# Optimization experiments

Measured on AMD Instinct MI355X. Metric: run time of the kernel, lower is better.

The kernel has to match this reference:

```python
import jax, jax.numpy as jnp
import numpy as np

LN_EPS = 1e-5
SA_EPS = 1e-8
NUM_ITERS = 3

def layer_norm(x, w, b):
    mu = jnp.mean(x, axis=-1, keepdims=True)
    var = jnp.mean((x - mu) ** 2, axis=-1, keepdims=True)
    return (x - mu) / jnp.sqrt(var + LN_EPS) * w + b


def setup_inputs() -> dict:
    key = jax.random.key(0)
    ks = jax.random.split(key, 24)
    B, C, H, W = 128, 256, 32, 32
    D, S, MH, NC = 64, 8, 128, 15
    s = lambda k, shape, scale=0.02: jax.random.normal(k, shape, dtype=jnp.float32) * scale
    inp = {
        "x1": jax.random.normal(ks[0], (B, C, H, W), dtype=jnp.float32),
        "x2": jax.random.normal(ks[1], (B, C, H, W), dtype=jnp.float32),
        # 1x1 convs stored as [out,in]
        "conv1_w": s(ks[2], (D, C)), "conv1_b": jnp.zeros((D,), jnp.float32),
        "conv2_w": s(ks[3], (D, C)), "conv2_b": jnp.zeros((D,), jnp.float32),
        "norm_w": jnp.ones((D,), jnp.float32), "norm_b": jnp.zeros((D,), jnp.float32),
        "ni_w": jnp.ones((D,), jnp.float32), "ni_b": jnp.zeros((D,), jnp.float32),
        "ns_w": jnp.ones((D,), jnp.float32), "ns_b": jnp.zeros((D,), jnp.float32),
        "nm_w": jnp.ones((D,), jnp.float32), "nm_b": jnp.zeros((D,), jnp.float32),
        "slots_mu": s(ks[4], (1, 1, D), 1.0), "slots_log_sigma": s(ks[5], (1, 1, D), 0.1),
        "Wq": s(ks[6], (D, D), 0.1), "Wk": s(ks[7], (D, D), 0.1), "Wv": s(ks[8], (D, D), 0.1),
        "gru_wih": s(ks[9], (3 * D, D), 0.1), "gru_whh": s(ks[10], (3 * D, D), 0.1),
        "gru_bih": jnp.zeros((3 * D,), jnp.float32), "gru_bhh": jnp.zeros((3 * D,), jnp.float32),
        "mlp_w1": s(ks[11], (MH, D), 0.1), "mlp_b1": jnp.zeros((MH,), jnp.float32),
        "mlp_w2": s(ks[12], (D, MH), 0.1), "mlp_b2": jnp.zeros((D,), jnp.float32),
        "head_w": s(ks[13], (NC, D), 0.1), "head_b": jnp.zeros((NC,), jnp.float32),
        "noise": jax.random.normal(ks[14], (B, S, D), dtype=jnp.float32),
    }
    return inp


def _forward(x1, x2, conv1_w, conv1_b, conv2_w, conv2_b, norm_w, norm_b,
             ni_w, ni_b, ns_w, ns_b, nm_w, nm_b, slots_mu, slots_log_sigma,
             Wq, Wk, Wv, gru_wih, gru_whh, gru_bih, gru_bhh,
             mlp_w1, mlp_b1, mlp_w2, mlp_b2, head_w, head_b, noise):
    B = x1.shape[0]
    D = Wq.shape[0]
    # 1x1 convs then flatten to tokens: [B, H*W, D]
    t1 = jnp.einsum('bchw,dc->bhwd', x1, conv1_w).reshape(B, -1, D) + conv1_b
    t2 = jnp.einsum('bchw,dc->bhwd', x2, conv2_w).reshape(B, -1, D) + conv2_b
    inputs = jnp.concatenate([t1, t2], axis=1)          # [B, N, D]
    inputs = layer_norm(inputs, norm_w, norm_b)

    # SlotAttention
    inputs = layer_norm(inputs, ni_w, ni_b)
    k = inputs @ Wk.T                                    # [B, N, D]
    v = inputs @ Wv.T
    slots = slots_mu + jnp.exp(slots_log_sigma) * noise  # [B, S, D]
    scale = D ** -0.5
    for _ in range(NUM_ITERS):
        slots_prev = slots
        sn = layer_norm(slots, ns_w, ns_b)
        q = (sn @ Wq.T) * scale                          # [B, S, D]
        attn_logits = jnp.einsum('bnd,bsd->bns', k, q)   # [B, N, S]
        attn = jax.nn.softmax(attn_logits, axis=-1) + SA_EPS
        attn = attn / jnp.sum(attn, axis=-2, keepdims=True)
        updates = jnp.einsum('bns,bnd->bsd', attn, v)    # [B, S, D]
        # GRUCell (torch gate order: r, z, n)
        gi = updates @ gru_wih.T + gru_bih               # [B, S, 3D]
        gh = slots_prev @ gru_whh.T + gru_bhh
        ir, iz, inn = jnp.split(gi, 3, axis=-1)
        hr, hz, hn = jnp.split(gh, 3, axis=-1)
        r = jax.nn.sigmoid(ir + hr)
        z = jax.nn.sigmoid(iz + hz)
        n = jnp.tanh(inn + r * hn)
        slots = (1.0 - z) * n + z * slots_prev
        # residual MLP
        h = layer_norm(slots, nm_w, nm_b)
        h = jax.nn.relu(h @ mlp_w1.T + mlp_b1) @ mlp_w2.T + mlp_b2
        slots = slots + h

    fused = jnp.mean(slots, axis=1)                      # [B, D]
    return fused @ head_w.T + head_b                     # [B, n_classes]


def reference(x1, x2, conv1_w, conv1_b, conv2_w, conv2_b, norm_w, norm_b,
              ni_w, ni_b, ns_w, ns_b, nm_w, nm_b, slots_mu, slots_log_sigma,
              Wq, Wk, Wv, gru_wih, gru_whh, gru_bih, gru_bhh,
              mlp_w1, mlp_b1, mlp_w2, mlp_b2, head_w, head_b, noise):
    return _forward(x1, x2, conv1_w, conv1_b, conv2_w, conv2_b, norm_w, norm_b,
                    ni_w, ni_b, ns_w, ns_b, nm_w, nm_b, slots_mu, slots_log_sigma,
                    Wq, Wk, Wv, gru_wih, gru_whh, gru_bih, gru_bhh,
                    mlp_w1, mlp_b1, mlp_w2, mlp_b2, head_w, head_b, noise)
```

## Files before the change

kernel.cpp:

```cpp
#include <hip/hip_runtime.h>
#include <stdint.h>


typedef __bf16 bf16;
typedef __bf16 bf16x8 __attribute__((ext_vector_type(8)));
typedef float  f32x4  __attribute__((ext_vector_type(4)));

#define MFMA16(a, b, c) __builtin_amdgcn_mfma_f32_16x16x32_bf16((a), (b), (c), 0, 0, 0)

#define ASYNC_LDS16(g, l) \
  __builtin_amdgcn_global_load_lds((const __attribute__((address_space(1))) void*)(g), \
                                   (__attribute__((address_space(3))) void*)(l), 16, 0, 0)

__global__ __launch_bounds__(256) void k0_convert(
    const float* __restrict__ c1w, const float* __restrict__ c2w,
    const float* __restrict__ wk,  const float* __restrict__ wvv,
    bf16* __restrict__ wconv, bf16* __restrict__ wkv)
{
  const int i = blockIdx.x * 256 + threadIdx.x;
  if (i < 16384) {
    wconv[i]         = (bf16)c1w[i];
    wconv[16384 + i] = (bf16)c2w[i];
  }
  if (i < 4096) {
    wkv[i]        = (bf16)wk[i];
    wkv[4096 + i] = (bf16)wvv[i];
  }
}

__global__ __launch_bounds__(256) void k1_conv_kv(
    const float* __restrict__ x1, const float* __restrict__ x2,
    const float* __restrict__ c1b, const float* __restrict__ c2b,
    const float* __restrict__ nw,  const float* __restrict__ nb,
    const float* __restrict__ niw, const float* __restrict__ nib,
    const bf16* __restrict__ wconv, const bf16* __restrict__ wkv,
    bf16* __restrict__ kbuf, bf16* __restrict__ vT)
{
  __shared__ union {
    float xs[32 * 264];
    struct { float T[64][65]; bf16 tok[64][72]; } p2;
    struct { float Tk[64][65]; float Tv[64][65]; } kv;
  } U;

  const int bx   = blockIdx.x;
  const int tile = bx & 15;
  const int img  = (bx >> 4) & 1;
  const int b    = bx >> 5;
  const int tid  = threadIdx.x;
  const int lane = tid & 63;
  const int wvid = tid >> 6;
  const int l15  = lane & 15;
  const int quad = lane >> 4;

  const float* xp  = (img ? x2 : x1) + (size_t)b * (256 * 1024) + tile * 64;
  const int   rowin = lane >> 4;
  const int   pq    = (lane & 15) * 4;
  const float* ga0  = xp + (size_t)rowin * 1024 + pq;
  const bf16* wc = wconv + img * (64 * 256);
  const int p = wvid * 16 + l15;

  f32x4 acc[4] = {{0.f,0.f,0.f,0.f},{0.f,0.f,0.f,0.f},{0.f,0.f,0.f,0.f},{0.f,0.f,0.f,0.f}};

  for (int half = 0; half < 2; ++half) {
    #pragma unroll
    for (int gi = 0; gi < 8; ++gi) {
      const int g = wvid + gi * 4;
      ASYNC_LDS16(ga0 + (size_t)(half * 128 + g * 4) * 1024, &U.xs[g * 264]);
    }
    __syncthreads();
    #pragma unroll
    for (int k0 = 0; k0 < 128; k0 += 32) {
      bf16x8 af;
      #pragma unroll
      for (int j = 0; j < 8; ++j) {
        const int c = k0 + quad * 8 + j;
        af[j] = (bf16)U.xs[(c >> 2) * 264 + (c & 3) * 64 + p];
      }
      #pragma unroll
      for (int nt = 0; nt < 4; ++nt) {
        const bf16x8 bw = *(const bf16x8*)&wc[(nt * 16 + l15) * 256 + half * 128 + k0 + quad * 8];
        acc[nt] = MFMA16(af, bw, acc[nt]);
      }
    }
    __syncthreads();
  }

  {
    const float* cb = img ? c2b : c1b;
    #pragma unroll
    for (int nt = 0; nt < 4; ++nt) {
      const int d = nt * 16 + l15;
      const float bias = cb[d];
      #pragma unroll
      for (int r = 0; r < 4; ++r)
        U.p2.T[wvid * 16 + quad * 4 + r][d] = acc[nt][r] + bias;
    }
  }
  __syncthreads();

  {
    const int pix = tid >> 2, part = tid & 3;
    float xv[16], yv[16];
    float s = 0.f, s2 = 0.f;
    #pragma unroll
    for (int i = 0; i < 16; ++i) {
      xv[i] = U.p2.T[pix][part * 16 + i];
      s += xv[i]; s2 += xv[i] * xv[i];
    }
    s  += __shfl_xor(s, 1);  s  += __shfl_xor(s, 2);
    s2 += __shfl_xor(s2, 1); s2 += __shfl_xor(s2, 2);
    float mu   = s * 0.015625f;
    float rstd = rsqrtf(s2 * 0.015625f - mu * mu + 1e-5f);
    s = 0.f; s2 = 0.f;
    #pragma unroll
    for (int i = 0; i < 16; ++i) {
      const int d = part * 16 + i;
      const float y = (xv[i] - mu) * rstd * nw[d] + nb[d];
      yv[i] = y; s += y; s2 += y * y;
    }
    s  += __shfl_xor(s, 1);  s  += __shfl_xor(s, 2);
    s2 += __shfl_xor(s2, 1); s2 += __shfl_xor(s2, 2);
    mu   = s * 0.015625f;
    rstd = rsqrtf(s2 * 0.015625f - mu * mu + 1e-5f);
    #pragma unroll
    for (int i = 0; i < 16; ++i) {
      const int d = part * 16 + i;
      U.p2.tok[pix][d] = (bf16)((yv[i] - mu) * rstd * niw[d] + nib[d]);
    }
  }
  __syncthreads();

  f32x4 ak[4] = {{0.f,0.f,0.f,0.f},{0.f,0.f,0.f,0.f},{0.f,0.f,0.f,0.f},{0.f,0.f,0.f,0.f}};
  f32x4 av[4] = {{0.f,0.f,0.f,0.f},{0.f,0.f,0.f,0.f},{0.f,0.f,0.f,0.f},{0.f,0.f,0.f,0.f}};
  #pragma unroll
  for (int k0 = 0; k0 < 64; k0 += 32) {
    const bf16x8 af = *(const bf16x8*)&U.p2.tok[wvid * 16 + l15][k0 + quad * 8];
    #pragma unroll
    for (int nt = 0; nt < 4; ++nt) {
      const bf16x8 bk = *(const bf16x8*)&wkv[(nt * 16 + l15) * 64 + k0 + quad * 8];
      const bf16x8 bv = *(const bf16x8*)&wkv[4096 + (nt * 16 + l15) * 64 + k0 + quad * 8];
      ak[nt] = MFMA16(af, bk, ak[nt]);
      av[nt] = MFMA16(af, bv, av[nt]);
    }
  }
  __syncthreads();

  #pragma unroll
  for (int nt = 0; nt < 4; ++nt)
    #pragma unroll
    for (int r = 0; r < 4; ++r) {
      U.kv.Tk[wvid * 16 + quad * 4 + r][nt * 16 + l15] = ak[nt][r];
      U.kv.Tv[nt * 16 + l15][wvid * 16 + quad * 4 + r] = av[nt][r];
    }
  __syncthreads();
  {
    const int row = tid >> 2, dd = (tid & 3) * 16;
    const size_t kb = ((size_t)b * 2048 + img * 1024 + tile * 64) * 64;
    bf16 tb[16];
    #pragma unroll
    for (int i = 0; i < 16; ++i) tb[i] = (bf16)U.kv.Tk[row][dd + i];
    *(bf16x8*)&kbuf[kb + (size_t)row * 64 + dd]     = *(bf16x8*)&tb[0];
    *(bf16x8*)&kbuf[kb + (size_t)row * 64 + dd + 8] = *(bf16x8*)&tb[8];
    #pragma unroll
    for (int i = 0; i < 16; ++i) tb[i] = (bf16)U.kv.Tv[row][dd + i];
    const size_t vb = ((size_t)b * 64 + row) * 2048 + img * 1024 + tile * 64 + dd;
    *(bf16x8*)&vT[vb]     = *(bf16x8*)&tb[0];
    *(bf16x8*)&vT[vb + 8] = *(bf16x8*)&tb[8];
  }
}

__global__ __launch_bounds__(512) void kS0(
    const float* __restrict__ smu, const float* __restrict__ slog,
    const float* __restrict__ noise,
    const float* __restrict__ nsw, const float* __restrict__ nsb,
    const float* __restrict__ Wq,
    float* __restrict__ slotbuf, bf16* __restrict__ qbuf)
{
  __shared__ float tmp[8][66];
  const int b = blockIdx.x, tid = threadIdx.x;
  const int s0 = tid >> 6, d0 = tid & 63;
  const int part = tid & 7, sl = (tid >> 3) & 7, wv = tid >> 6;

  const float sval = smu[d0] + expf(slog[d0]) * noise[((size_t)b * 8 + s0) * 64 + d0];
  slotbuf[((size_t)b * 8 + s0) * 64 + d0] = sval;
  float s = sval, s2 = sval * sval;
  #pragma unroll
  for (int m = 1; m < 64; m <<= 1) { s += __shfl_xor(s, m); s2 += __shfl_xor(s2, m); }
  const float mu = s * 0.015625f;
  const float rstd = rsqrtf(s2 * 0.015625f - mu * mu + 1e-5f);
  tmp[s0][d0] = (sval - mu) * rstd * nsw[d0] + nsb[d0];
  __syncthreads();

  float tm[8];
  #pragma unroll
  for (int i = 0; i < 8; ++i) tm[i] = tmp[sl][part * 8 + i];
  for (int orr = 0; orr < 8; ++orr) {
    const int d = orr * 8 + wv;
    const f32x4 w0 = *(const f32x4*)&Wq[d * 64 + part * 8];
    const f32x4 w1v = *(const f32x4*)&Wq[d * 64 + part * 8 + 4];
    float a = tm[0]*w0[0] + tm[1]*w0[1] + tm[2]*w0[2] + tm[3]*w0[3]
            + tm[4]*w1v[0] + tm[5]*w1v[1] + tm[6]*w1v[2] + tm[7]*w1v[3];
    a += __shfl_xor(a, 1); a += __shfl_xor(a, 2); a += __shfl_xor(a, 4);
    if (part == 0) qbuf[((size_t)b * 8 + sl) * 64 + d] = (bf16)(a * 0.125f);
  }
}

__global__ __launch_bounds__(256) void kA(
    const bf16* __restrict__ kbuf, const bf16* __restrict__ vT,
    const bf16* __restrict__ qbuf,
    float* __restrict__ updpart, float* __restrict__ colpart)
{
  __shared__ bf16  qs[16][72];
  __shared__ bf16  attn_b[16][136];
  __shared__ float updp[4][8][64];
  __shared__ float cspart[4][8];

  const int bx  = blockIdx.x;
  const int b   = bx >> 4, ch = bx & 15;
  const int tid = threadIdx.x;
  const int lane = tid & 63, wvid = tid >> 6;
  const int l15 = lane & 15, quad = lane >> 4;
  const size_t tokbase = (size_t)b * 2048 + ch * 128;

  if (tid < 64) {
    const int s = tid >> 3, o = (tid & 7) * 8;
    *(bf16x8*)&qs[s][o] = *(const bf16x8*)&qbuf[((size_t)b * 8 + s) * 64 + o];
  } else if (tid < 128) {
    const int s = 8 + ((tid - 64) >> 3), o = ((tid - 64) & 7) * 8;
    uint32_t* zp = (uint32_t*)&qs[s][o];
    zp[0] = 0u; zp[1] = 0u; zp[2] = 0u; zp[3] = 0u;
  }
  {
    uint32_t* az = (uint32_t*)&attn_b[8][0];
    for (int i = tid; i < 544; i += 256) az[i] = 0u;
  }
  __syncthreads();

  {
    float cs = 0.f;
    #pragma unroll
    for (int mt = 0; mt < 2; ++mt) {
      const int t0 = wvid * 32 + mt * 16;
      const bf16* kr = kbuf + (tokbase + t0 + l15) * 64 + quad * 8;
      f32x4 lg = {0.f, 0.f, 0.f, 0.f};
      lg = MFMA16(*(const bf16x8*)&kr[0],  *(const bf16x8*)&qs[l15][quad * 8],      lg);
      lg = MFMA16(*(const bf16x8*)&kr[32], *(const bf16x8*)&qs[l15][32 + quad * 8], lg);
      #pragma unroll
      for (int r = 0; r < 4; ++r) {
        const float l = lg[r];
        float m = l;
        m = fmaxf(m, __shfl_xor(m, 1));
        m = fmaxf(m, __shfl_xor(m, 2));
        m = fmaxf(m, __shfl_xor(m, 4));
        const float e = expf(l - m);
        float ss = e;
        ss += __shfl_xor(ss, 1);
        ss += __shfl_xor(ss, 2);
        ss += __shfl_xor(ss, 4);
        const float at = e / ss + 1e-8f;
        if (l15 < 8) {
          const bf16 ab = (bf16)at;
          attn_b[l15][t0 + quad * 4 + r] = ab;
          cs += (float)ab;
        }
      }
    }
    cs += __shfl_xor(cs, 16);
    cs += __shfl_xor(cs, 32);
    if (lane < 8) cspart[wvid][lane] = cs;
  }
  __syncthreads();

  {
    const bf16x8 afr = *(const bf16x8*)&attn_b[l15][wvid * 32 + quad * 8];
    const bf16* vrow = vT + (size_t)b * 131072 + (size_t)ch * 128 + wvid * 32 + quad * 8;
    const f32x4 zero4 = {0.f, 0.f, 0.f, 0.f};
    #pragma unroll
    for (int nt = 0; nt < 4; ++nt) {
      const bf16x8 bv = *(const bf16x8*)&vrow[(size_t)(nt * 16 + l15) * 2048];
      f32x4 dd = MFMA16(afr, bv, zero4);
      if (quad < 2) {
        #pragma unroll
        for (int r = 0; r < 4; ++r)
          updp[wvid][quad * 4 + r][nt * 16 + l15] = dd[r];
      }
    }
  }
  __syncthreads();

  {
    const float* up = &updp[0][0][0];
    float* og = updpart + ((size_t)b * 16 + ch) * 512;
    for (int o = tid; o < 512; o += 256)
      og[o] = up[o] + up[o + 512] + up[o + 1024] + up[o + 1536];
    if (tid < 8)
      colpart[((size_t)b * 16 + ch) * 8 + tid] =
        cspart[0][tid] + cspart[1][tid] + cspart[2][tid] + cspart[3][tid];
  }
}

__global__ __launch_bounds__(512) void kB(
    const float* __restrict__ updpart, const float* __restrict__ colpart,
    float* __restrict__ slotbuf, bf16* __restrict__ qbuf,
    const float* __restrict__ nsw, const float* __restrict__ nsb,
    const float* __restrict__ nmw, const float* __restrict__ nmb,
    const float* __restrict__ Wq,
    const float* __restrict__ wih, const float* __restrict__ whh,
    const float* __restrict__ bih, const float* __restrict__ bhh,
    const float* __restrict__ w1,  const float* __restrict__ b1,
    const float* __restrict__ w2,  const float* __restrict__ b2,
    const float* __restrict__ hwt, const float* __restrict__ hb,
    float* __restrict__ out, const int last)
{
  __shared__ float slots[8][66];
  __shared__ float tmp[8][66];
  __shared__ float gig[8][192], ghg[8][192];
  __shared__ float h1[8][132];
  const int b = blockIdx.x, tid = threadIdx.x;
  const int s0 = tid >> 6, d0 = tid & 63;
  const int part = tid & 7, sl = (tid >> 3) & 7, wv = tid >> 6;

  {
    const float* up = updpart + (size_t)b * 8192 + s0 * 64 + d0;
    float u = 0.f;
    #pragma unroll
    for (int ch = 0; ch < 16; ++ch) u += up[ch * 512];
    const float* cp = colpart + (size_t)b * 128 + s0;
    float cs = 0.f;
    #pragma unroll
    for (int ch = 0; ch < 16; ++ch) cs += cp[ch * 8];
    tmp[s0][d0] = u / cs;
    slots[s0][d0] = slotbuf[((size_t)b * 8 + s0) * 64 + d0];
  }
  __syncthreads();

  {
    float tv[8], sv[8];
    #pragma unroll
    for (int i = 0; i < 8; ++i) { tv[i] = tmp[sl][part * 8 + i]; sv[i] = slots[sl][part * 8 + i]; }
    for (int jr = 0; jr < 24; ++jr) {
      const int j = jr * 8 + wv;
      const f32x4 wa0 = *(const f32x4*)&wih[j * 64 + part * 8];
      const f32x4 wa1 = *(const f32x4*)&wih[j * 64 + part * 8 + 4];
      const f32x4 wb0 = *(const f32x4*)&whh[j * 64 + part * 8];
      const f32x4 wb1 = *(const f32x4*)&whh[j * 64 + part * 8 + 4];
      float a = tv[0]*wa0[0] + tv[1]*wa0[1] + tv[2]*wa0[2] + tv[3]*wa0[3]
              + tv[4]*wa1[0] + tv[5]*wa1[1] + tv[6]*wa1[2] + tv[7]*wa1[3];
      float h = sv[0]*wb0[0] + sv[1]*wb0[1] + sv[2]*wb0[2] + sv[3]*wb0[3]
              + sv[4]*wb1[0] + sv[5]*wb1[1] + sv[6]*wb1[2] + sv[7]*wb1[3];
      a += __shfl_xor(a, 1); a += __shfl_xor(a, 2); a += __shfl_xor(a, 4);
      h += __shfl_xor(h, 1); h += __shfl_xor(h, 2); h += __shfl_xor(h, 4);
      if (part == 0) { gig[sl][j] = a + bih[j]; ghg[sl][j] = h + bhh[j]; }
    }
  }
  __syncthreads();

  float snew;
  {
    const float r  = 1.f / (1.f + expf(-(gig[s0][d0]       + ghg[s0][d0])));
    const float z  = 1.f / (1.f + expf(-(gig[s0][64 + d0]  + ghg[s0][64 + d0])));
    const float nn = tanhf(gig[s0][128 + d0] + r * ghg[s0][128 + d0]);
    snew = (1.f - z) * nn + z * slots[s0][d0];
    slots[s0][d0] = snew;
  }
  {
    float s = snew, s2 = snew * snew;
    #pragma unroll
    for (int m = 1; m < 64; m <<= 1) { s += __shfl_xor(s, m); s2 += __shfl_xor(s2, m); }
    const float mu = s * 0.015625f;
    const float rstd = rsqrtf(s2 * 0.015625f - mu * mu + 1e-5f);
    tmp[s0][d0] = (snew - mu) * rstd * nmw[d0] + nmb[d0];
  }
  __syncthreads();

  {
    float tm[8];
    #pragma unroll
    for (int i = 0; i < 8; ++i) tm[i] = tmp[sl][part * 8 + i];
    for (int jr = 0; jr < 16; ++jr) {
      const int j = jr * 8 + wv;
      const f32x4 w0 = *(const f32x4*)&w1[j * 64 + part * 8];
      const f32x4 w1v = *(const f32x4*)&w1[j * 64 + part * 8 + 4];
      float a = tm[0]*w0[0] + tm[1]*w0[1] + tm[2]*w0[2] + tm[3]*w0[3]
              + tm[4]*w1v[0] + tm[5]*w1v[1] + tm[6]*w1v[2] + tm[7]*w1v[3];
      a += __shfl_xor(a, 1); a += __shfl_xor(a, 2); a += __shfl_xor(a, 4);
      if (part == 0) h1[sl][j] = fmaxf(a + b1[j], 0.f);
    }
  }
  __syncthreads();

  for (int orr = 0; orr < 8; ++orr) {
    const int d = orr * 8 + wv;
    float a = 0.f;
    #pragma unroll
    for (int i = 0; i < 4; ++i) {
      const f32x4 wv4 = *(const f32x4*)&w2[d * 128 + part * 16 + i * 4];
      a += h1[sl][part * 16 + i * 4 + 0] * wv4[0] + h1[sl][part * 16 + i * 4 + 1] * wv4[1]
         + h1[sl][part * 16 + i * 4 + 2] * wv4[2] + h1[sl][part * 16 + i * 4 + 3] * wv4[3];
    }
    a += __shfl_xor(a, 1); a += __shfl_xor(a, 2); a += __shfl_xor(a, 4);
    if (part == 0) slots[sl][d] += a + b2[d];
  }
  __syncthreads();

  const float sfin = slots[s0][d0];
  slotbuf[((size_t)b * 8 + s0) * 64 + d0] = sfin;

  if (!last) {
    float s = sfin, s2 = sfin * sfin;
    #pragma unroll
    for (int m = 1; m < 64; m <<= 1) { s += __shfl_xor(s, m); s2 += __shfl_xor(s2, m); }
    const float mu = s * 0.015625f;
    const float rstd = rsqrtf(s2 * 0.015625f - mu * mu + 1e-5f);
    tmp[s0][d0] = (sfin - mu) * rstd * nsw[d0] + nsb[d0];
    __syncthreads();
    float tm[8];
    #pragma unroll
    for (int i = 0; i < 8; ++i) tm[i] = tmp[sl][part * 8 + i];
    for (int orr = 0; orr < 8; ++orr) {
      const int d = orr * 8 + wv;
      const f32x4 w0 = *(const f32x4*)&Wq[d * 64 + part * 8];
      const f32x4 w1v = *(const f32x4*)&Wq[d * 64 + part * 8 + 4];
      float a = tm[0]*w0[0] + tm[1]*w0[1] + tm[2]*w0[2] + tm[3]*w0[3]
              + tm[4]*w1v[0] + tm[5]*w1v[1] + tm[6]*w1v[2] + tm[7]*w1v[3];
      a += __shfl_xor(a, 1); a += __shfl_xor(a, 2); a += __shfl_xor(a, 4);
      if (part == 0) qbuf[((size_t)b * 8 + sl) * 64 + d] = (bf16)(a * 0.125f);
    }
  } else {
    if (tid < 64) {
      float f = 0.f;
      #pragma unroll
      for (int s = 0; s < 8; ++s) f += slots[s][tid];
      tmp[0][tid] = f * 0.125f;
    }
    __syncthreads();
    if (tid < 15) {
      float a = hb[tid];
      for (int d = 0; d < 64; ++d) a += tmp[0][d] * hwt[tid * 64 + d];
      out[b * 15 + tid] = a;
    }
  }
}

extern "C" void kernel_launch(void* const* d_in, const int* in_sizes, int n_in,
                              void* d_out, int out_size, void* d_ws, size_t ws_size,
                              hipStream_t stream) {
  const float* x1   = (const float*)d_in[0];
  const float* x2   = (const float*)d_in[1];
  const float* c1w  = (const float*)d_in[2];
  const float* c1b  = (const float*)d_in[3];
  const float* c2w  = (const float*)d_in[4];
  const float* c2b  = (const float*)d_in[5];
  const float* nw   = (const float*)d_in[6];
  const float* nb   = (const float*)d_in[7];
  const float* niw  = (const float*)d_in[8];
  const float* nib  = (const float*)d_in[9];
  const float* nsw  = (const float*)d_in[10];
  const float* nsb  = (const float*)d_in[11];
  const float* nmw  = (const float*)d_in[12];
  const float* nmb  = (const float*)d_in[13];
  const float* smu  = (const float*)d_in[14];
  const float* slog = (const float*)d_in[15];
  const float* Wq   = (const float*)d_in[16];
  const float* Wk   = (const float*)d_in[17];
  const float* Wv   = (const float*)d_in[18];
  const float* wih  = (const float*)d_in[19];
  const float* whh  = (const float*)d_in[20];
  const float* bih  = (const float*)d_in[21];
  const float* bhh  = (const float*)d_in[22];
  const float* w1   = (const float*)d_in[23];
  const float* b1   = (const float*)d_in[24];
  const float* w2   = (const float*)d_in[25];
  const float* b2   = (const float*)d_in[26];
  const float* hwt  = (const float*)d_in[27];
  const float* hb   = (const float*)d_in[28];
  const float* noise= (const float*)d_in[29];

  char* ws = (char*)d_ws;
  bf16*  kbuf    = (bf16*)(ws);
  bf16*  vT      = (bf16*)(ws + (size_t)33554432);
  bf16*  wconv   = (bf16*)(ws + (size_t)67108864);
  bf16*  wkv     = (bf16*)(ws + (size_t)67174400);
  float* slotbuf = (float*)(ws + (size_t)67190784);
  bf16*  qbuf    = (bf16*)(ws + (size_t)67452928);
  float* updpart = (float*)(ws + (size_t)67584000);
  float* colpart = (float*)(ws + (size_t)71778304);

  k0_convert<<<dim3(64), dim3(256), 0, stream>>>(c1w, c2w, Wk, Wv, wconv, wkv);
  k1_conv_kv<<<dim3(4096), dim3(256), 0, stream>>>(x1, x2, c1b, c2b, nw, nb, niw, nib,
                                                   wconv, wkv, kbuf, vT);
  kS0<<<dim3(128), dim3(512), 0, stream>>>(smu, slog, noise, nsw, nsb, Wq, slotbuf, qbuf);
  for (int it = 0; it < 3; ++it) {
    kA<<<dim3(2048), dim3(256), 0, stream>>>(kbuf, vT, qbuf, updpart, colpart);
    kB<<<dim3(128), dim3(512), 0, stream>>>(updpart, colpart, slotbuf, qbuf,
                                            nsw, nsb, nmw, nmb, Wq,
                                            wih, whh, bih, bhh, w1, b1, w2, b2,
                                            hwt, hb, (float*)d_out, (it == 2) ? 1 : 0);
  }
}
```

Before: 523.9 us.

## Fuse slot GRU/MLP update into attention kernel and shrink conv LDS footprint

The per-iteration slot update kernel is removed. Each of the 16 attention blocks per batch now recomputes the GRU, MLP, LayerNorm and Q projection redundantly from the reduced partials, with ping-pong buffers between launches and a small final kernel for the head. This cuts the launch count and serial small-grid kernels, at the cost of the same scalar GRU work being repeated by 16 blocks per batch, and it stores update partials in bf16. The conv kernel also stages 32 input channels per step instead of 128 and reuses one LDS buffer for the K and V transposes, reducing shared memory so more blocks can be resident.

```diff
diff --git a/kernel.cpp b/kernel.cpp
--- a/kernel.cpp
+++ b/kernel.cpp
@@ -11,6 +11,12 @@
 #define ASYNC_LDS16(g, l) \
   __builtin_amdgcn_global_load_lds((const __attribute__((address_space(1))) void*)(g), \
                                    (__attribute__((address_space(3))) void*)(l), 16, 0, 0)
+
+union Scr {
+  struct { float sr[8][64], sz[8][64], inn[8][64], hn[8][64]; } g;
+  float h1[8][132];
+  float updp[4][8][64];
+};
 
 __global__ __launch_bounds__(256) void k0_convert(
     const float* __restrict__ c1w, const float* __restrict__ c2w,
@@ -37,9 +43,9 @@
     bf16* __restrict__ kbuf, bf16* __restrict__ vT)
 {
   __shared__ union {
-    float xs[32 * 264];
-    struct { float T[64][65]; bf16 tok[64][72]; } p2;
-    struct { float Tk[64][65]; float Tv[64][65]; } kv;
+    float xs[8 * 264];
+    float T[64][65];
+    bf16  tok[64][72];
   } U;
 
   const int bx   = blockIdx.x;
@@ -52,35 +58,32 @@
   const int l15  = lane & 15;
   const int quad = lane >> 4;
 
-  const float* xp  = (img ? x2 : x1) + (size_t)b * (256 * 1024) + tile * 64;
+  const float* xp   = (img ? x2 : x1) + (size_t)b * (256 * 1024) + tile * 64;
   const int   rowin = lane >> 4;
   const int   pq    = (lane & 15) * 4;
   const float* ga0  = xp + (size_t)rowin * 1024 + pq;
-  const bf16* wc = wconv + img * (64 * 256);
+  const bf16* wc    = wconv + img * (64 * 256);
   const int p = wvid * 16 + l15;
 
   f32x4 acc[4] = {{0.f,0.f,0.f,0.f},{0.f,0.f,0.f,0.f},{0.f,0.f,0.f,0.f},{0.f,0.f,0.f,0.f}};
 
-  for (int half = 0; half < 2; ++half) {
-    #pragma unroll
-    for (int gi = 0; gi < 8; ++gi) {
-      const int g = wvid + gi * 4;
-      ASYNC_LDS16(ga0 + (size_t)(half * 128 + g * 4) * 1024, &U.xs[g * 264]);
+  for (int step = 0; step < 8; ++step) {
+    #pragma unroll
+    for (int gi = 0; gi < 2; ++gi) {
+      const int g = wvid * 2 + gi;
+      ASYNC_LDS16(ga0 + (size_t)(step * 32 + g * 4) * 1024, &U.xs[g * 264]);
     }
     __syncthreads();
-    #pragma unroll
-    for (int k0 = 0; k0 < 128; k0 += 32) {
-      bf16x8 af;
-      #pragma unroll
-      for (int j = 0; j < 8; ++j) {
-        const int c = k0 + quad * 8 + j;
-        af[j] = (bf16)U.xs[(c >> 2) * 264 + (c & 3) * 64 + p];
-      }
-      #pragma unroll
-      for (int nt = 0; nt < 4; ++nt) {
-        const bf16x8 bw = *(const bf16x8*)&wc[(nt * 16 + l15) * 256 + half * 128 + k0 + quad * 8];
-        acc[nt] = MFMA16(af, bw, acc[nt]);
-      }
+    bf16x8 af;
+    #pragma unroll
+    for (int j = 0; j < 8; ++j) {
+      const int cl = quad * 8 + j;
+      af[j] = (bf16)U.xs[(cl >> 2) * 264 + (cl & 3) * 64 + p];
+    }
+    #pragma unroll
+    for (int nt = 0; nt < 4; ++nt) {
+      const bf16x8 bw = *(const bf16x8*)&wc[(nt * 16 + l15) * 256 + step * 32 + quad * 8];
+      acc[nt] = MFMA16(af, bw, acc[nt]);
     }
     __syncthreads();
   }
@@ -93,18 +96,19 @@
       const float bias = cb[d];
       #pragma unroll
       for (int r = 0; r < 4; ++r)
-        U.p2.T[wvid * 16 + quad * 4 + r][d] = acc[nt][r] + bias;
-    }
-  }
-  __syncthreads();
-
+        U.T[wvid * 16 + quad * 4 + r][d] = acc[nt][r] + bias;
+    }
+  }
+  __syncthreads();
+
+  float yv[16];
   {
     const int pix = tid >> 2, part = tid & 3;
-    float xv[16], yv[16];
+    float xv[16];
     float s = 0.f, s2 = 0.f;
     #pragma unroll
     for (int i = 0; i < 16; ++i) {
-      xv[i] = U.p2.T[pix][part * 16 + i];
+      xv[i] = U.T[pix][part * 16 + i];
       s += xv[i]; s2 += xv[i] * xv[i];
     }
     s  += __shfl_xor(s, 1);  s  += __shfl_xor(s, 2);
@@ -125,8 +129,14 @@
     #pragma unroll
     for (int i = 0; i < 16; ++i) {
       const int d = part * 16 + i;
-      U.p2.tok[pix][d] = (bf16)((yv[i] - mu) * rstd * niw[d] + nib[d]);
-    }
+      yv[i] = (yv[i] - mu) * rstd * niw[d] + nib[d];
+    }
+  }
+  __syncthreads();
+  {
+    const int pix = tid >> 2, part = tid & 3;
+    #pragma unroll
+    for (int i = 0; i < 16; ++i) U.tok[pix][part * 16 + i] = (bf16)yv[i];
   }
   __syncthreads();
 
@@ -134,7 +144,7 @@
   f32x4 av[4] = {{0.f,0.f,0.f,0.f},{0.f,0.f,0.f,0.f},{0.f,0.f,0.f,0.f},{0.f,0.f,0.f,0.f}};
   #pragma unroll
   for (int k0 = 0; k0 < 64; k0 += 32) {
-    const bf16x8 af = *(const bf16x8*)&U.p2.tok[wvid * 16 + l15][k0 + quad * 8];
+    const bf16x8 af = *(const bf16x8*)&U.tok[wvid * 16 + l15][k0 + quad * 8];
     #pragma unroll
     for (int nt = 0; nt < 4; ++nt) {
       const bf16x8 bk = *(const bf16x8*)&wkv[(nt * 16 + l15) * 64 + k0 + quad * 8];
@@ -148,71 +158,175 @@
   #pragma unroll
   for (int nt = 0; nt < 4; ++nt)
     #pragma unroll
-    for (int r = 0; r < 4; ++r) {
-      U.kv.Tk[wvid * 16 + quad * 4 + r][nt * 16 + l15] = ak[nt][r];
-      U.kv.Tv[nt * 16 + l15][wvid * 16 + quad * 4 + r] = av[nt][r];
-    }
+    for (int r = 0; r < 4; ++r)
+      U.T[wvid * 16 + quad * 4 + r][nt * 16 + l15] = ak[nt][r];
   __syncthreads();
   {
     const int row = tid >> 2, dd = (tid & 3) * 16;
     const size_t kb = ((size_t)b * 2048 + img * 1024 + tile * 64) * 64;
     bf16 tb[16];
     #pragma unroll
-    for (int i = 0; i < 16; ++i) tb[i] = (bf16)U.kv.Tk[row][dd + i];
+    for (int i = 0; i < 16; ++i) tb[i] = (bf16)U.T[row][dd + i];
     *(bf16x8*)&kbuf[kb + (size_t)row * 64 + dd]     = *(bf16x8*)&tb[0];
     *(bf16x8*)&kbuf[kb + (size_t)row * 64 + dd + 8] = *(bf16x8*)&tb[8];
-    #pragma unroll
-    for (int i = 0; i < 16; ++i) tb[i] = (bf16)U.kv.Tv[row][dd + i];
+  }
+  __syncthreads();
+  #pragma unroll
+  for (int nt = 0; nt < 4; ++nt)
+    #pragma unroll
+    for (int r = 0; r < 4; ++r)
+      U.T[nt * 16 + l15][wvid * 16 + quad * 4 + r] = av[nt][r];
+  __syncthreads();
+  {
+    const int row = tid >> 2, dd = (tid & 3) * 16;
+    bf16 tb[16];
+    #pragma unroll
+    for (int i = 0; i < 16; ++i) tb[i] = (bf16)U.T[row][dd + i];
     const size_t vb = ((size_t)b * 64 + row) * 2048 + img * 1024 + tile * 64 + dd;
     *(bf16x8*)&vT[vb]     = *(bf16x8*)&tb[0];
     *(bf16x8*)&vT[vb + 8] = *(bf16x8*)&tb[8];
   }
 }
 
-__global__ __launch_bounds__(512) void kS0(
-    const float* __restrict__ smu, const float* __restrict__ slog,
-    const float* __restrict__ noise,
+
+__device__ __forceinline__ void gru_mlp_update(
+    int tid, float (*slots)[66], float (*tmp)[66], Scr* scr,
+    const float* __restrict__ wih, const float* __restrict__ whh,
+    const float* __restrict__ bih, const float* __restrict__ bhh,
+    const float* __restrict__ w1,  const float* __restrict__ b1,
+    const float* __restrict__ w2,  const float* __restrict__ b2,
+    const float* __restrict__ nmw, const float* __restrict__ nmb)
+{
+  const int lane = tid & 63, wv = tid >> 6;
+  const int part = lane & 7, sl = lane >> 3;
+
+  {
+    float tv[8], sv[8];
+    #pragma unroll
+    for (int i = 0; i < 8; ++i) { tv[i] = tmp[sl][part * 8 + i]; sv[i] = slots[sl][part * 8 + i]; }
+    for (int jr = 0; jr < 48; ++jr) {
+      const int j = jr * 4 + wv;
+      const f32x4 wa0 = *(const f32x4*)&wih[j * 64 + part * 8];
+      const f32x4 wa1 = *(const f32x4*)&wih[j * 64 + part * 8 + 4];
+      const f32x4 wb0 = *(const f32x4*)&whh[j * 64 + part * 8];
+      const f32x4 wb1 = *(const f32x4*)&whh[j * 64 + part * 8 + 4];
+      float a = tv[0]*wa0[0] + tv[1]*wa0[1] + tv[2]*wa0[2] + tv[3]*wa0[3]
+              + tv[4]*wa1[0] + tv[5]*wa1[1] + tv[6]*wa1[2] + tv[7]*wa1[3];
+      float h = sv[0]*wb0[0] + sv[1]*wb0[1] + sv[2]*wb0[2] + sv[3]*wb0[3]
+              + sv[4]*wb1[0] + sv[5]*wb1[1] + sv[6]*wb1[2] + sv[7]*wb1[3];
+      a += __shfl_xor(a, 1); a += __shfl_xor(a, 2); a += __shfl_xor(a, 4);
+      h += __shfl_xor(h, 1); h += __shfl_xor(h, 2); h += __shfl_xor(h, 4);
+      if (part == 0) {
+        const float gi_ = a + bih[j], gh_ = h + bhh[j];
+        if (j < 64)       scr->g.sr[sl][j] = gi_ + gh_;
+        else if (j < 128) scr->g.sz[sl][j - 64] = gi_ + gh_;
+        else { scr->g.inn[sl][j - 128] = gi_; scr->g.hn[sl][j - 128] = gh_; }
+      }
+    }
+  }
+  __syncthreads();
+  for (int i = tid; i < 512; i += 256) {
+    const int s = i >> 6, d = i & 63;
+    const float r  = 1.f / (1.f + expf(-scr->g.sr[s][d]));
+    const float z  = 1.f / (1.f + expf(-scr->g.sz[s][d]));
+    const float nn = tanhf(scr->g.inn[s][d] + r * scr->g.hn[s][d]);
+    slots[s][d] = (1.f - z) * nn + z * slots[s][d];
+  }
+  __syncthreads();
+  for (int rr = wv; rr < 8; rr += 4) {
+    const float v = slots[rr][lane];
+    float s = v, s2 = v * v;
+    #pragma unroll
+    for (int m = 1; m < 64; m <<= 1) { s += __shfl_xor(s, m); s2 += __shfl_xor(s2, m); }
+    const float mu = s * 0.015625f;
+    const float rstd = rsqrtf(s2 * 0.015625f - mu * mu + 1e-5f);
+    tmp[rr][lane] = (v - mu) * rstd * nmw[lane] + nmb[lane];
+  }
+  __syncthreads();
+  {
+    float tm[8];
+    #pragma unroll
+    for (int i = 0; i < 8; ++i) tm[i] = tmp[sl][part * 8 + i];
+    for (int jr = 0; jr < 32; ++jr) {
+      const int j = jr * 4 + wv;
+      const f32x4 w0 = *(const f32x4*)&w1[j * 64 + part * 8];
+      const f32x4 w1v = *(const f32x4*)&w1[j * 64 + part * 8 + 4];
+      float a = tm[0]*w0[0] + tm[1]*w0[1] + tm[2]*w0[2] + tm[3]*w0[3]
+              + tm[4]*w1v[0] + tm[5]*w1v[1] + tm[6]*w1v[2] + tm[7]*w1v[3];
+      a += __shfl_xor(a, 1); a += __shfl_xor(a, 2); a += __shfl_xor(a, 4);
+      if (part == 0) scr->h1[sl][j] = fmaxf(a + b1[j], 0.f);
+    }
+  }
+  __syncthreads();
+  for (int orr = 0; orr < 16; ++orr) {
+    const int d = orr * 4 + wv;
+    float a = 0.f;
+    #pragma unroll
+    for (int i = 0; i < 4; ++i) {
+      const f32x4 wv4 = *(const f32x4*)&w2[d * 128 + part * 16 + i * 4];
+      a += scr->h1[sl][part * 16 + i * 4 + 0] * wv4[0] + scr->h1[sl][part * 16 + i * 4 + 1] * wv4[1]
+         + scr->h1[sl][part * 16 + i * 4 + 2] * wv4[2] + scr->h1[sl][part * 16 + i * 4 + 3] * wv4[3];
+    }
+    a += __shfl_xor(a, 1); a += __shfl_xor(a, 2); a += __shfl_xor(a, 4);
+    if (part == 0) slots[sl][d] += a + b2[d];
+  }
+  __syncthreads();
+}
+
+__device__ __forceinline__ void ln_q(
+    int tid, float (*slots)[66], float (*tmp)[66],
     const float* __restrict__ nsw, const float* __restrict__ nsb,
-    const float* __restrict__ Wq,
-    float* __restrict__ slotbuf, bf16* __restrict__ qbuf)
+    const float* __restrict__ Wq, bf16 (*qs)[72])
 {
-  __shared__ float tmp[8][66];
-  const int b = blockIdx.x, tid = threadIdx.x;
-  const int s0 = tid >> 6, d0 = tid & 63;
-  const int part = tid & 7, sl = (tid >> 3) & 7, wv = tid >> 6;
-
-  const float sval = smu[d0] + expf(slog[d0]) * noise[((size_t)b * 8 + s0) * 64 + d0];
-  slotbuf[((size_t)b * 8 + s0) * 64 + d0] = sval;
-  float s = sval, s2 = sval * sval;
-  #pragma unroll
-  for (int m = 1; m < 64; m <<= 1) { s += __shfl_xor(s, m); s2 += __shfl_xor(s2, m); }
-  const float mu = s * 0.015625f;
-  const float rstd = rsqrtf(s2 * 0.015625f - mu * mu + 1e-5f);
-  tmp[s0][d0] = (sval - mu) * rstd * nsw[d0] + nsb[d0];
-  __syncthreads();
-
+  const int lane = tid & 63, wv = tid >> 6;
+  const int part = lane & 7, sl = lane >> 3;
+  for (int rr = wv; rr < 8; rr += 4) {
+    const float v = slots[rr][lane];
+    float s = v, s2 = v * v;
+    #pragma unroll
+    for (int m = 1; m < 64; m <<= 1) { s += __shfl_xor(s, m); s2 += __shfl_xor(s2, m); }
+    const float mu = s * 0.015625f;
+    const float rstd = rsqrtf(s2 * 0.015625f - mu * mu + 1e-5f);
+    tmp[rr][lane] = (v - mu) * rstd * nsw[lane] + nsb[lane];
+  }
+  __syncthreads();
   float tm[8];
   #pragma unroll
   for (int i = 0; i < 8; ++i) tm[i] = tmp[sl][part * 8 + i];
-  for (int orr = 0; orr < 8; ++orr) {
-    const int d = orr * 8 + wv;
+  for (int orr = 0; orr < 16; ++orr) {
+    const int d = orr * 4 + wv;
     const f32x4 w0 = *(const f32x4*)&Wq[d * 64 + part * 8];
     const f32x4 w1v = *(const f32x4*)&Wq[d * 64 + part * 8 + 4];
     float a = tm[0]*w0[0] + tm[1]*w0[1] + tm[2]*w0[2] + tm[3]*w0[3]
             + tm[4]*w1v[0] + tm[5]*w1v[1] + tm[6]*w1v[2] + tm[7]*w1v[3];
     a += __shfl_xor(a, 1); a += __shfl_xor(a, 2); a += __shfl_xor(a, 4);
-    if (part == 0) qbuf[((size_t)b * 8 + sl) * 64 + d] = (bf16)(a * 0.125f);
-  }
+    if (part == 0) qs[sl][d] = (bf16)(a * 0.125f);
+  }
+  __syncthreads();
 }
 
 __global__ __launch_bounds__(256) void kA(
+    const int mode,
     const bf16* __restrict__ kbuf, const bf16* __restrict__ vT,
-    const bf16* __restrict__ qbuf,
-    float* __restrict__ updpart, float* __restrict__ colpart)
+    const float* __restrict__ smu, const float* __restrict__ slog,
+    const float* __restrict__ noise,
+    const float* __restrict__ nsw, const float* __restrict__ nsb,
+    const float* __restrict__ nmw, const float* __restrict__ nmb,
+    const float* __restrict__ Wq,
+    const float* __restrict__ wih, const float* __restrict__ whh,
+    const float* __restrict__ bih, const float* __restrict__ bhh,
+    const float* __restrict__ w1,  const float* __restrict__ b1,
+    const float* __restrict__ w2,  const float* __restrict__ b2,
+    const float* __restrict__ sbIn, float* __restrict__ sbOut,
+    const bf16* __restrict__ updIn, bf16* __restrict__ updOut,
+    const float* __restrict__ colIn, float* __restrict__ colOut)
 {
+  __shared__ float sl_slots[8][66];
+  __shared__ float sl_tmp[8][66];
+  __shared__ float sl_colsum[8];
+  __shared__ Scr   scr;
   __shared__ bf16  qs[16][72];
   __shared__ bf16  attn_b[16][136];
-  __shared__ float updp[4][8][64];
   __shared__ float cspart[4][8];
 
   const int bx  = blockIdx.x;
@@ -222,19 +336,48 @@
   const int l15 = lane & 15, quad = lane >> 4;
   const size_t tokbase = (size_t)b * 2048 + ch * 128;
 
-  if (tid < 64) {
-    const int s = tid >> 3, o = (tid & 7) * 8;
-    *(bf16x8*)&qs[s][o] = *(const bf16x8*)&qbuf[((size_t)b * 8 + s) * 64 + o];
-  } else if (tid < 128) {
-    const int s = 8 + ((tid - 64) >> 3), o = ((tid - 64) & 7) * 8;
-    uint32_t* zp = (uint32_t*)&qs[s][o];
-    zp[0] = 0u; zp[1] = 0u; zp[2] = 0u; zp[3] = 0u;
-  }
-  {
-    uint32_t* az = (uint32_t*)&attn_b[8][0];
-    for (int i = tid; i < 544; i += 256) az[i] = 0u;
-  }
-  __syncthreads();
+  for (int i = tid; i < 544; i += 256) ((uint32_t*)&attn_b[8][0])[i] = 0u;
+  { const int r8 = 8 + (tid >> 5), c2 = tid & 31; *(uint32_t*)&qs[r8][c2 * 2] = 0u; }
+
+  if (mode == 0) {
+    for (int i = tid; i < 512; i += 256) {
+      const int s = i >> 6, d = i & 63;
+      const float sv = smu[d] + expf(slog[d]) * noise[(size_t)b * 512 + i];
+      sl_slots[s][d] = sv;
+      if (ch == 0) sbOut[(size_t)b * 512 + i] = sv;
+    }
+    __syncthreads();
+  } else {
+    if (tid < 8) {
+      float cs = 0.f;
+      #pragma unroll
+      for (int c = 0; c < 16; ++c) cs += colIn[(size_t)b * 128 + c * 8 + tid];
+      sl_colsum[tid] = cs;
+    }
+    float u[2];
+    #pragma unroll
+    for (int t = 0; t < 2; ++t) {
+      const int i = tid + t * 256;
+      float uu = 0.f;
+      #pragma unroll
+      for (int c = 0; c < 16; ++c) uu += (float)updIn[(size_t)b * 8192 + c * 512 + i];
+      u[t] = uu;
+      sl_slots[i >> 6][i & 63] = sbIn[(size_t)b * 512 + i];
+    }
+    __syncthreads();
+    #pragma unroll
+    for (int t = 0; t < 2; ++t) {
+      const int i = tid + t * 256;
+      sl_tmp[i >> 6][i & 63] = u[t] / sl_colsum[i >> 6];
+    }
+    __syncthreads();
+    gru_mlp_update(tid, sl_slots, sl_tmp, &scr, wih, whh, bih, bhh,
+                   w1, b1, w2, b2, nmw, nmb);
+    if (ch == 0)
+      for (int i = tid; i < 512; i += 256)
+        sbOut[(size_t)b * 512 + i] = sl_slots[i >> 6][i & 63];
+  }
+  ln_q(tid, sl_slots, sl_tmp, nsw, nsb, Wq, qs);
 
   {
     float cs = 0.f;
@@ -282,163 +425,77 @@
       if (quad < 2) {
         #pragma unroll
         for (int r = 0; r < 4; ++r)
-          updp[wvid][quad * 4 + r][nt * 16 + l15] = dd[r];
+          scr.updp[wvid][quad * 4 + r][nt * 16 + l15] = dd[r];
       }
     }
   }
   __syncthreads();
-
-  {
-    const float* up = &updp[0][0][0];
-    float* og = updpart + ((size_t)b * 16 + ch) * 512;
+  {
+    const float* up = &scr.updp[0][0][0];
+    bf16* og = updOut + ((size_t)b * 16 + ch) * 512;
     for (int o = tid; o < 512; o += 256)
-      og[o] = up[o] + up[o + 512] + up[o + 1024] + up[o + 1536];
+      og[o] = (bf16)(up[o] + up[o + 512] + up[o + 1024] + up[o + 1536]);
     if (tid < 8)
-      colpart[((size_t)b * 16 + ch) * 8 + tid] =
+      colOut[((size_t)b * 16 + ch) * 8 + tid] =
         cspart[0][tid] + cspart[1][tid] + cspart[2][tid] + cspart[3][tid];
   }
 }
 
-__global__ __launch_bounds__(512) void kB(
-    const float* __restrict__ updpart, const float* __restrict__ colpart,
-    float* __restrict__ slotbuf, bf16* __restrict__ qbuf,
-    const float* __restrict__ nsw, const float* __restrict__ nsb,
-    const float* __restrict__ nmw, const float* __restrict__ nmb,
-    const float* __restrict__ Wq,
+__global__ __launch_bounds__(256) void kBfin(
+    const float* __restrict__ sbIn,
+    const bf16* __restrict__ updIn, const float* __restrict__ colIn,
     const float* __restrict__ wih, const float* __restrict__ whh,
     const float* __restrict__ bih, const float* __restrict__ bhh,
     const float* __restrict__ w1,  const float* __restrict__ b1,
     const float* __restrict__ w2,  const float* __restrict__ b2,
+    const float* __restrict__ nmw, const float* __restrict__ nmb,
     const float* __restrict__ hwt, const float* __restrict__ hb,
-    float* __restrict__ out, const int last)
+    float* __restrict__ out)
 {
-  __shared__ float slots[8][66];
-  __shared__ float tmp[8][66];
-  __shared__ float gig[8][192], ghg[8][192];
-  __shared__ float h1[8][132];
+  __shared__ float sl_slots[8][66];
+  __shared__ float sl_tmp[8][66];
+  __shared__ float sl_colsum[8];
+  __shared__ Scr   scr;
+
   const int b = blockIdx.x, tid = threadIdx.x;
-  const int s0 = tid >> 6, d0 = tid & 63;
-  const int part = tid & 7, sl = (tid >> 3) & 7, wv = tid >> 6;
-
-  {
-    const float* up = updpart + (size_t)b * 8192 + s0 * 64 + d0;
-    float u = 0.f;
-    #pragma unroll
-    for (int ch = 0; ch < 16; ++ch) u += up[ch * 512];
-    const float* cp = colpart + (size_t)b * 128 + s0;
+
+  if (tid < 8) {
     float cs = 0.f;
     #pragma unroll
-    for (int ch = 0; ch < 16; ++ch) cs += cp[ch * 8];
-    tmp[s0][d0] = u / cs;
-    slots[s0][d0] = slotbuf[((size_t)b * 8 + s0) * 64 + d0];
-  }
-  __syncthreads();
-
-  {
-    float tv[8], sv[8];
-    #pragma unroll
-    for (int i = 0; i < 8; ++i) { tv[i] = tmp[sl][part * 8 + i]; sv[i] = slots[sl][part * 8 + i]; }
-    for (int jr = 0; jr < 24; ++jr) {
-      const int j = jr * 8 + wv;
-      const f32x4 wa0 = *(const f32x4*)&wih[j * 64 + part * 8];
-      const f32x4 wa1 = *(const f32x4*)&wih[j * 64 + part * 8 + 4];
-      const f32x4 wb0 = *(const f32x4*)&whh[j * 64 + part * 8];
-      const f32x4 wb1 = *(const f32x4*)&whh[j * 64 + part * 8 + 4];
-      float a = tv[0]*wa0[0] + tv[1]*wa0[1] + tv[2]*wa0[2] + tv[3]*wa0[3]
-              + tv[4]*wa1[0] + tv[5]*wa1[1] + tv[6]*wa1[2] + tv[7]*wa1[3];
-      float h = sv[0]*wb0[0] + sv[1]*wb0[1] + sv[2]*wb0[2] + sv[3]*wb0[3]
-              + sv[4]*wb1[0] + sv[5]*wb1[1] + sv[6]*wb1[2] + sv[7]*wb1[3];
-      a += __shfl_xor(a, 1); a += __shfl_xor(a, 2); a += __shfl_xor(a, 4);
-      h += __shfl_xor(h, 1); h += __shfl_xor(h, 2); h += __shfl_xor(h, 4);
-      if (part == 0) { gig[sl][j] = a + bih[j]; ghg[sl][j] = h + bhh[j]; }
-    }
-  }
-  __syncthreads();
-
-  float snew;
-  {
-    const float r  = 1.f / (1.f + expf(-(gig[s0][d0]       + ghg[s0][d0])));
-    const float z  = 1.f / (1.f + expf(-(gig[s0][64 + d0]  + ghg[s0][64 + d0])));
-    const float nn = tanhf(gig[s0][128 + d0] + r * ghg[s0][128 + d0]);
-    snew = (1.f - z) * nn + z * slots[s0][d0];
-    slots[s0][d0] = snew;
-  }
-  {
-    float s = snew, s2 = snew * snew;
-    #pragma unroll
-    for (int m = 1; m < 64; m <<= 1) { s += __shfl_xor(s, m); s2 += __shfl_xor(s2, m); }
-    const float mu = s * 0.015625f;
-    const float rstd = rsqrtf(s2 * 0.015625f - mu * mu + 1e-5f);
-    tmp[s0][d0] = (snew - mu) * rstd * nmw[d0] + nmb[d0];
-  }
-  __syncthreads();
-
-  {
-    float tm[8];
-    #pragma unroll
-    for (int i = 0; i < 8; ++i) tm[i] = tmp[sl][part * 8 + i];
-    for (int jr = 0; jr < 16; ++jr) {
-      const int j = jr * 8 + wv;
-      const f32x4 w0 = *(const f32x4*)&w1[j * 64 + part * 8];
-      const f32x4 w1v = *(const f32x4*)&w1[j * 64 + part * 8 + 4];
-      float a = tm[0]*w0[0] + tm[1]*w0[1] + tm[2]*w0[2] + tm[3]*w0[3]
-              + tm[4]*w1v[0] + tm[5]*w1v[1] + tm[6]*w1v[2] + tm[7]*w1v[3];
-      a += __shfl_xor(a, 1); a += __shfl_xor(a, 2); a += __shfl_xor(a, 4);
-      if (part == 0) h1[sl][j] = fmaxf(a + b1[j], 0.f);
-    }
-  }
-  __syncthreads();
-
-  for (int orr = 0; orr < 8; ++orr) {
-    const int d = orr * 8 + wv;
-    float a = 0.f;
-    #pragma unroll
-    for (int i = 0; i < 4; ++i) {
-      const f32x4 wv4 = *(const f32x4*)&w2[d * 128 + part * 16 + i * 4];
-      a += h1[sl][part * 16 + i * 4 + 0] * wv4[0] + h1[sl][part * 16 + i * 4 + 1] * wv4[1]
-         + h1[sl][part * 16 + i * 4 + 2] * wv4[2] + h1[sl][part * 16 + i * 4 + 3] * wv4[3];
-    }
-    a += __shfl_xor(a, 1); a += __shfl_xor(a, 2); a += __shfl_xor(a, 4);
-    if (part == 0) slots[sl][d] += a + b2[d];
-  }
-  __syncthreads();
-
-  const float sfin = slots[s0][d0];
-  slotbuf[((size_t)b * 8 + s0) * 64 + d0] = sfin;
-
-  if (!last) {
-    float s = sfin, s2 = sfin * sfin;
-    #pragma unroll
-    for (int m = 1; m < 64; m <<= 1) { s += __shfl_xor(s, m); s2 += __shfl_xor(s2, m); }
-    const float mu = s * 0.015625f;
-    const float rstd = rsqrtf(s2 * 0.015625f - mu * mu + 1e-5f);
-    tmp[s0][d0] = (sfin - mu) * rstd * nsw[d0] + nsb[d0];
-    __syncthreads();
-    float tm[8];
-    #pragma unroll
-    for (int i = 0; i < 8; ++i) tm[i] = tmp[sl][part * 8 + i];
-    for (int orr = 0; orr < 8; ++orr) {
-      const int d = orr * 8 + wv;
-      const f32x4 w0 = *(const f32x4*)&Wq[d * 64 + part * 8];
-      const f32x4 w1v = *(const f32x4*)&Wq[d * 64 + part * 8 + 4];
-      float a = tm[0]*w0[0] + tm[1]*w0[1] + tm[2]*w0[2] + tm[3]*w0[3]
-              + tm[4]*w1v[0] + tm[5]*w1v[1] + tm[6]*w1v[2] + tm[7]*w1v[3];
-      a += __shfl_xor(a, 1); a += __shfl_xor(a, 2); a += __shfl_xor(a, 4);
-      if (part == 0) qbuf[((size_t)b * 8 + sl) * 64 + d] = (bf16)(a * 0.125f);
-    }
-  } else {
-    if (tid < 64) {
-      float f = 0.f;
-      #pragma unroll
-      for (int s = 0; s < 8; ++s) f += slots[s][tid];
-      tmp[0][tid] = f * 0.125f;
-    }
-    __syncthreads();
-    if (tid < 15) {
-      float a = hb[tid];
-      for (int d = 0; d < 64; ++d) a += tmp[0][d] * hwt[tid * 64 + d];
-      out[b * 15 + tid] = a;
-    }
+    for (int c = 0; c < 16; ++c) cs += colIn[(size_t)b * 128 + c * 8 + tid];
+    sl_colsum[tid] = cs;
+  }
+  float u[2];
+  #pragma unroll
+  for (int t = 0; t < 2; ++t) {
+    const int i = tid + t * 256;
+    float uu = 0.f;
+    #pragma unroll
+    for (int c = 0; c < 16; ++c) uu += (float)updIn[(size_t)b * 8192 + c * 512 + i];
+    u[t] = uu;
+    sl_slots[i >> 6][i & 63] = sbIn[(size_t)b * 512 + i];
+  }
+  __syncthreads();
+  #pragma unroll
+  for (int t = 0; t < 2; ++t) {
+    const int i = tid + t * 256;
+    sl_tmp[i >> 6][i & 63] = u[t] / sl_colsum[i >> 6];
+  }
+  __syncthreads();
+  gru_mlp_update(tid, sl_slots, sl_tmp, &scr, wih, whh, bih, bhh,
+                 w1, b1, w2, b2, nmw, nmb);
+
+  if (tid < 64) {
+    float f = 0.f;
+    #pragma unroll
+    for (int s = 0; s < 8; ++s) f += sl_slots[s][tid];
+    sl_tmp[0][tid] = f * 0.125f;
+  }
+  __syncthreads();
+  if (tid < 15) {
+    float a = hb[tid];
+    for (int d = 0; d < 64; ++d) a += sl_tmp[0][d] * hwt[tid * 64 + d];
+    out[b * 15 + tid] = a;
   }
 }
 
@@ -477,24 +534,29 @@
   const float* noise= (const float*)d_in[29];
 
   char* ws = (char*)d_ws;
-  bf16*  kbuf    = (bf16*)(ws);
-  bf16*  vT      = (bf16*)(ws + (size_t)33554432);
-  bf16*  wconv   = (bf16*)(ws + (size_t)67108864);
-  bf16*  wkv     = (bf16*)(ws + (size_t)67174400);
-  float* slotbuf = (float*)(ws + (size_t)67190784);
-  bf16*  qbuf    = (bf16*)(ws + (size_t)67452928);
-  float* updpart = (float*)(ws + (size_t)67584000);
-  float* colpart = (float*)(ws + (size_t)71778304);
+  bf16*  kbuf  = (bf16*)(ws);
+  bf16*  vT    = (bf16*)(ws + (size_t)33554432);
+  bf16*  wconv = (bf16*)(ws + (size_t)67108864);
+  bf16*  wkv   = (bf16*)(ws + (size_t)67174400);
+  float* sb0   = (float*)(ws + (size_t)67190784);
+  float* sb1   = (float*)(ws + (size_t)67452928);
+  bf16*  updA  = (bf16*)(ws + (size_t)67715072);
+  bf16*  updB  = (bf16*)(ws + (size_t)69812224);
+  float* colA  = (float*)(ws + (size_t)71909376);
+  float* colB  = (float*)(ws + (size_t)71974912);
 
   k0_convert<<<dim3(64), dim3(256), 0, stream>>>(c1w, c2w, Wk, Wv, wconv, wkv);
   k1_conv_kv<<<dim3(4096), dim3(256), 0, stream>>>(x1, x2, c1b, c2b, nw, nb, niw, nib,
                                                    wconv, wkv, kbuf, vT);
-  kS0<<<dim3(128), dim3(512), 0, stream>>>(smu, slog, noise, nsw, nsb, Wq, slotbuf, qbuf);
-  for (int it = 0; it < 3; ++it) {
-    kA<<<dim3(2048), dim3(256), 0, stream>>>(kbuf, vT, qbuf, updpart, colpart);
-    kB<<<dim3(128), dim3(512), 0, stream>>>(updpart, colpart, slotbuf, qbuf,
-                                            nsw, nsb, nmw, nmb, Wq,
-                                            wih, whh, bih, bhh, w1, b1, w2, b2,
-                                            hwt, hb, (float*)d_out, (it == 2) ? 1 : 0);
-  }
-}
+  kA<<<dim3(2048), dim3(256), 0, stream>>>(0, kbuf, vT, smu, slog, noise,
+      nsw, nsb, nmw, nmb, Wq, wih, whh, bih, bhh, w1, b1, w2, b2,
+      nullptr, sb0, nullptr, updA, nullptr, colA);
+  kA<<<dim3(2048), dim3(256), 0, stream>>>(1, kbuf, vT, smu, slog, noise,
+      nsw, nsb, nmw, nmb, Wq, wih, whh, bih, bhh, w1, b1, w2, b2,
+      sb0, sb1, updA, updB, colA, colB);
+  kA<<<dim3(2048), dim3(256), 0, stream>>>(1, kbuf, vT, smu, slog, noise,
+      nsw, nsb, nmw, nmb, Wq, wih, whh, bih, bhh, w1, b1, w2, b2,
+      sb1, sb0, updB, updA, colB, colA);
+  kBfin<<<dim3(128), dim3(256), 0, stream>>>(sb0, updA, colA,
+      wih, whh, bih, bhh, w1, b1, w2, b2, nmw, nmb, hwt, hb, (float*)d_out);
+}
```

Measured after the change: 757.4 us. 44.6% more time.
